# Optimization experiments

Hardware: AMD Instinct MI355X
Metric: run time of the kernel (lower is better)

## Reference

```python
import jax, jax.numpy as jnp
import numpy as np

EPS = 1e-08
K_N = 10
K_E = 10
F_DIM = 512
SCALE = F_DIM ** -0.5
N_NODES = 16384
N_EDGES = 2048


def layernorm(x, w, b):
    mu = x.mean(axis=-1, keepdims=True)
    var = x.var(axis=-1, keepdims=True)
    return (x - mu) * jax.lax.rsqrt(var + 1e-5) * w + b


def mask_attn(attn, k):
    # topk along last dim, scatter boolean mask, elementwise masking
    _, idx = jax.lax.top_k(attn, k)
    rows = jnp.arange(attn.shape[0])[:, None]
    mask = jnp.zeros(attn.shape, dtype=bool).at[rows, idx].set(True)
    return attn * mask


def setup_inputs() -> dict:
    key = jax.random.key(0)
    ks = jax.random.split(key, 12)
    d, h = F_DIM, 512  # hidden = max(f_dim, 128)
    w = 0.02  # weight init scale to keep softmax unsaturated
    return {
        'inputs': jax.random.normal(ks[0], (N_NODES, d), jnp.float32),
        'noise': jax.random.normal(ks[1], (N_EDGES, d), jnp.float32),
        'edges_mu': jax.random.normal(ks[2], (1, d), jnp.float32),
        'edges_logsigma': jnp.zeros((1, d), jnp.float32),
        'Wq': jax.random.normal(ks[3], (d, d), jnp.float32) * w,
        'bq': jnp.zeros((d,), jnp.float32),
        'Wk': jax.random.normal(ks[4], (d, d), jnp.float32) * w,
        'bk': jnp.zeros((d,), jnp.float32),
        'Wv': jax.random.normal(ks[5], (d, d), jnp.float32) * w,
        'bv': jnp.zeros((d,), jnp.float32),
        'W1': jax.random.normal(ks[6], (2 * d, h), jnp.float32) * w,
        'b1': jnp.zeros((h,), jnp.float32),
        'W2': jax.random.normal(ks[7], (h, d), jnp.float32) * w,
        'b2': jnp.zeros((d,), jnp.float32),
        'ln_in_w': jnp.ones((d,), jnp.float32),
        'ln_in_b': jnp.zeros((d,), jnp.float32),
        'ln_e_w': jnp.ones((d,), jnp.float32),
        'ln_e_b': jnp.zeros((d,), jnp.float32),
    }


def reference(inputs, noise, edges_mu, edges_logsigma, Wq, bq, Wk, bk, Wv, bv,
              W1, b1, W2, b2, ln_in_w, ln_in_b, ln_e_w, ln_e_b):
    relu = jax.nn.relu
    # slot init: mu + sigma * noise  -> [n_s, d]
    edges = edges_mu + jnp.exp(edges_logsigma) * noise
    x = layernorm(inputs, ln_in_w, ln_in_b)          # [n, d]
    k = relu(x @ Wk + bk)                            # [n, d]
    v = relu(x @ Wv + bv)                            # [n, d]
    # single iteration (iters=1)
    e = layernorm(edges, ln_e_w, ln_e_b)             # [n_s, d]
    q = relu(e @ Wq + bq)                            # [n_s, d]
    dots = (q @ k.T) * SCALE                         # [n_s, n]
    attn = jax.nn.softmax(dots, axis=1) + EPS
    attn = attn / attn.sum(axis=1, keepdims=True)
    attn = mask_attn(attn, K_N)
    updates = attn @ v                               # [n_s, d]
    e = jnp.concatenate([e, updates], axis=1)        # [n_s, 2d]
    e = relu(e @ W1 + b1) @ W2 + b2                  # mlp -> [n_s, d]
    q2 = x @ Wq + bq                                 # note: no activation here
    k2 = relu(e @ Wk + bk)                           # [n_s, d]
    dots2 = (q2 @ k2.T) * SCALE                      # [n, n_s]
    attn_v = jax.nn.softmax(dots2, axis=1)
    H = mask_attn(attn_v, K_E)
    return e, H, dots2
```

## Files before the change

kernel.cpp:

```cpp
#include <hip/hip_runtime.h>
#include <stdint.h>


#define NN 16384
#define NE 2048
#define TOPK 10

static const float SCALE_F = 0.04419417382415922f;
#define EPS_F 1e-8f

using bf16x8  = __attribute__((ext_vector_type(8))) __bf16;
using floatx4 = __attribute__((ext_vector_type(4))) float;

__device__ __forceinline__ unsigned f_as_u(float f) {
  union { float f; unsigned u; } v; v.f = f; return v.u;
}
__device__ __forceinline__ float u_as_f(unsigned u) {
  union { unsigned u; float f; } v; v.u = u; return v.f;
}
__device__ __forceinline__ unsigned short f2bf(float f) {
  unsigned u = f_as_u(f);
  unsigned r = u + 0x7fffu + ((u >> 16) & 1u);
  return (unsigned short)(r >> 16);
}
__device__ __forceinline__ float bf2f(unsigned short h) {
  return u_as_f(((unsigned)h) << 16);
}

__device__ __forceinline__ void glds16(const unsigned short* g, unsigned short* l) {
  __builtin_amdgcn_global_load_lds(
      (const __attribute__((address_space(1))) unsigned int*)g,
      (__attribute__((address_space(3))) unsigned int*)l, 16, 0, 0);
}

__device__ __forceinline__ unsigned fkey(float f) {
  unsigned u = f_as_u(f);
  return (u & 0x80000000u) ? ~u : (u | 0x80000000u);
}
__device__ __forceinline__ float funkey(unsigned k) {
  unsigned u = (k & 0x80000000u) ? (k ^ 0x80000000u) : ~k;
  return u_as_f(u);
}
__device__ __forceinline__ unsigned long long packkc(float v, int col) {
  return ((unsigned long long)fkey(v) << 32) | (unsigned)(~(unsigned)col);
}
__device__ __forceinline__ int unpack_col(unsigned long long w) {
  return (int)(~(unsigned)(w & 0xFFFFFFFFull));
}
__device__ __forceinline__ float unpack_val(unsigned long long w) {
  return funkey((unsigned)(w >> 32));
}
__device__ __forceinline__ unsigned long long shfl_xor_u64(unsigned long long x, int m) {
  unsigned lo = (unsigned)x, hi = (unsigned)(x >> 32);
  lo = __shfl_xor(lo, m, 64);
  hi = __shfl_xor(hi, m, 64);
  return ((unsigned long long)hi << 32) | lo;
}

__global__ void transpose_cast_kernel(const float* __restrict__ src,
                                      unsigned short* __restrict__ dhi,
                                      unsigned short* __restrict__ dlo,
                                      int K, int N) {
  __shared__ float tile[32][33];
  int n0 = blockIdx.x * 32, k0 = blockIdx.y * 32;
  int tx = threadIdx.x, ty = threadIdx.y;
  for (int r = ty; r < 32; r += 8)
    tile[r][tx] = src[(size_t)(k0 + r) * N + n0 + tx];
  __syncthreads();
  for (int r = ty; r < 32; r += 8) {
    float v = tile[tx][r];
    size_t o = (size_t)(n0 + r) * K + k0 + tx;
    unsigned short h = f2bf(v);
    dhi[o] = h;
    if (dlo) dlo[o] = f2bf(v - bf2f(h));
  }
}

__global__ void transpose_cast3_kernel(const float* __restrict__ s0,
                                       const float* __restrict__ s1,
                                       const float* __restrict__ s2,
                                       unsigned short* __restrict__ dhi) {
  __shared__ float tile[32][33];
  const float* src = blockIdx.z == 0 ? s0 : (blockIdx.z == 1 ? s1 : s2);
  unsigned short* d = dhi + (size_t)blockIdx.z * 512 * 512;
  int n0 = blockIdx.x * 32, k0 = blockIdx.y * 32;
  int tx = threadIdx.x, ty = threadIdx.y;
  for (int r = ty; r < 32; r += 8)
    tile[r][tx] = src[(size_t)(k0 + r) * 512 + n0 + tx];
  __syncthreads();
  for (int r = ty; r < 32; r += 8)
    d[(size_t)(n0 + r) * 512 + k0 + tx] = f2bf(tile[tx][r]);
}

__device__ __forceinline__ float block_sum_256(float v, float* sm4) {
#pragma unroll
  for (int off = 32; off; off >>= 1) v += __shfl_down(v, off, 64);
  __syncthreads();
  if ((threadIdx.x & 63) == 0) sm4[threadIdx.x >> 6] = v;
  __syncthreads();
  return (sm4[0] + sm4[1]) + (sm4[2] + sm4[3]);
}

__global__ __launch_bounds__(256) void ln_x_kernel(
    const float* __restrict__ in, const float* __restrict__ w,
    const float* __restrict__ b, unsigned short* __restrict__ out_hi) {
  __shared__ float sm4[4];
  int row = blockIdx.x, tid = threadIdx.x;
  const float* r = in + (size_t)row * 512;
  float x0 = r[tid], x1 = r[tid + 256];
  float mu = block_sum_256(x0 + x1, sm4) * (1.0f / 512.0f);
  float d0 = x0 - mu, d1 = x1 - mu;
  float var = block_sum_256(d0 * d0 + d1 * d1, sm4) * (1.0f / 512.0f);
  float rs = rsqrtf(var + 1e-5f);
  out_hi[(size_t)row * 512 + tid]       = f2bf(d0 * rs * w[tid] + b[tid]);
  out_hi[(size_t)row * 512 + tid + 256] = f2bf(d1 * rs * w[tid + 256] + b[tid + 256]);
}

__global__ __launch_bounds__(256) void ln_e_kernel(
    const float* __restrict__ noise, const float* __restrict__ mu_e,
    const float* __restrict__ ls_e, const float* __restrict__ w,
    const float* __restrict__ b, unsigned short* __restrict__ e1_hi,
    unsigned short* __restrict__ e1_lo) {
  __shared__ float sm4[4];
  int row = blockIdx.x, tid = threadIdx.x;
  const float* r = noise + (size_t)row * 512;
  float x0 = mu_e[tid] + expf(ls_e[tid]) * r[tid];
  float x1 = mu_e[tid + 256] + expf(ls_e[tid + 256]) * r[tid + 256];
  float mu = block_sum_256(x0 + x1, sm4) * (1.0f / 512.0f);
  float d0 = x0 - mu, d1 = x1 - mu;
  float var = block_sum_256(d0 * d0 + d1 * d1, sm4) * (1.0f / 512.0f);
  float rs = rsqrtf(var + 1e-5f);
  float y0 = d0 * rs * w[tid] + b[tid];
  float y1 = d1 * rs * w[tid + 256] + b[tid + 256];
  size_t o = (size_t)row * 1024;
  unsigned short h0 = f2bf(y0), h1 = f2bf(y1);
  e1_hi[o + tid] = h0;             e1_lo[o + tid] = f2bf(y0 - bf2f(h0));
  e1_hi[o + tid + 256] = h1;       e1_lo[o + tid + 256] = f2bf(y1 - bf2f(h1));
}

#define GEMM128_CORE(A_, B_, bm_, bn_, acc_)                                   \
  __shared__ __align__(16) unsigned short As[128 * 32];                        \
  __shared__ __align__(16) unsigned short Bs[128 * 32];                        \
  {                                                                            \
    const unsigned short* gA0 = (A_) + ((bm_) + (tid >> 2)) * 512 + ((tid & 3) << 3); \
    const unsigned short* gA1 = gA0 + 64 * 512;                                \
    const unsigned short* gB0 = (B_) + ((bn_) + (tid >> 2)) * 512 + ((tid & 3) << 3); \
    const unsigned short* gB1 = gB0 + 64 * 512;                                \
    unsigned short* dA0 = &As[wave * 512];                                     \
    unsigned short* dA1 = &As[2048 + wave * 512];                              \
    unsigned short* dB0 = &Bs[wave * 512];                                     \
    unsigned short* dB1 = &Bs[2048 + wave * 512];                              \
    for (int k0 = 0; k0 < 512; k0 += 32) {                                     \
      glds16(gA0 + k0, dA0);                                                   \
      glds16(gA1 + k0, dA1);                                                   \
      glds16(gB0 + k0, dB0);                                                   \
      glds16(gB1 + k0, dB1);                                                   \
      __syncthreads();                                                         \
      bf16x8 af0 = *(const bf16x8*)&As[(wave * 32 + lrow) * 32 + quad * 8];    \
      bf16x8 af1 = *(const bf16x8*)&As[(wave * 32 + 16 + lrow) * 32 + quad * 8]; \
      _Pragma("unroll")                                                        \
      for (int t = 0; t < 8; ++t) {                                            \
        bf16x8 bfr = *(const bf16x8*)&Bs[(t * 16 + lrow) * 32 + quad * 8];     \
        acc_[0][t] = __builtin_amdgcn_mfma_f32_16x16x32_bf16(af0, bfr, acc_[0][t], 0, 0, 0); \
        acc_[1][t] = __builtin_amdgcn_mfma_f32_16x16x32_bf16(af1, bfr, acc_[1][t], 0, 0, 0); \
      }                                                                        \
      __syncthreads();                                                         \
    }                                                                          \
  }

__global__ __launch_bounds__(256) void gemm128_dots_kernel(
    const unsigned short* __restrict__ A, const unsigned short* __restrict__ B,
    float alpha, float* __restrict__ C, int ldc) {
  int tid = threadIdx.x, wave = tid >> 6, lane = tid & 63;
  int lrow = lane & 15, quad = lane >> 4;
  size_t bm = (size_t)blockIdx.x * 128, bn = (size_t)blockIdx.y * 128;
  floatx4 zero4 = {0.f, 0.f, 0.f, 0.f};
  floatx4 acc[2][8];
#pragma unroll
  for (int i = 0; i < 2; ++i)
#pragma unroll
    for (int t = 0; t < 8; ++t) acc[i][t] = zero4;
  GEMM128_CORE(A, B, bm, bn, acc)
#pragma unroll
  for (int i = 0; i < 2; ++i) {
    size_t row0 = bm + wave * 32 + i * 16 + quad * 4;
#pragma unroll
    for (int t = 0; t < 8; ++t) {
      int col = (int)bn + t * 16 + lrow;
#pragma unroll
      for (int r = 0; r < 4; ++r)
        C[(row0 + r) * (size_t)ldc + col] = acc[i][t][r] * alpha;
    }
  }
}

__global__ __launch_bounds__(256) void gemm128_kvq_kernel(
    const unsigned short* __restrict__ A, const unsigned short* __restrict__ B,
    const float* __restrict__ bk, const float* __restrict__ bv,
    const float* __restrict__ bq,
    unsigned short* __restrict__ khi, unsigned short* __restrict__ vhi,
    unsigned short* __restrict__ q2hi) {
  int tid = threadIdx.x, wave = tid >> 6, lane = tid & 63;
  int lrow = lane & 15, quad = lane >> 4;
  size_t bm = (size_t)blockIdx.x * 128, bn = (size_t)blockIdx.y * 128;
  floatx4 zero4 = {0.f, 0.f, 0.f, 0.f};
  floatx4 acc[2][8];
#pragma unroll
  for (int i = 0; i < 2; ++i)
#pragma unroll
    for (int t = 0; t < 8; ++t) acc[i][t] = zero4;
  GEMM128_CORE(A, B, bm, bn, acc)
  int mat = (int)(bn >> 9);
  int colbase = (int)(bn & 511);
  const float* bias = mat == 0 ? bk : (mat == 1 ? bv : bq);
  unsigned short* dst = mat == 0 ? khi : (mat == 1 ? vhi : q2hi);
  bool relu = mat < 2;
#pragma unroll
  for (int i = 0; i < 2; ++i) {
    size_t row0 = bm + wave * 32 + i * 16 + quad * 4;
#pragma unroll
    for (int t = 0; t < 8; ++t) {
      int col = colbase + t * 16 + lrow;
      float bvv = bias[col];
#pragma unroll
      for (int r = 0; r < 4; ++r) {
        float v = acc[i][t][r] + bvv;
        if (relu) v = fmaxf(v, 0.0f);
        dst[(row0 + r) * 512 + col] = f2bf(v);
      }
    }
  }
}

template <bool SPLIT, bool RELU, bool HAS_BIAS, bool WF32, bool WHI, bool WLO>
__global__ __launch_bounds__(256) void gemm64_kernel(
    const unsigned short* __restrict__ Ahi, const unsigned short* __restrict__ Alo, int lda,
    const unsigned short* __restrict__ Bhi, const unsigned short* __restrict__ Blo, int K,
    const float* __restrict__ bias, float alpha,
    float* __restrict__ Cf, int ldc,
    unsigned short* __restrict__ Chi, unsigned short* __restrict__ Clo, int ldcb) {
  __shared__ __align__(16) unsigned short AsH[64 * 32];
  __shared__ __align__(16) unsigned short BsH[64 * 32];
  __shared__ __align__(16) unsigned short AsL[64 * 32];
  __shared__ __align__(16) unsigned short BsL[64 * 32];
  int tid = threadIdx.x, wave = tid >> 6, lane = tid & 63;
  int lrow = lane & 15, quad = lane >> 4;
  size_t bm = (size_t)blockIdx.x * 64, bn = (size_t)blockIdx.y * 64;
  int row = tid >> 2, off = (tid & 3) << 3;
  size_t aoff = (bm + row) * (size_t)lda + off;
  size_t boff = (bn + row) * (size_t)K + off;

  floatx4 zero4 = {0.f, 0.f, 0.f, 0.f};
  floatx4 acc[4];
#pragma unroll
  for (int t = 0; t < 4; ++t) acc[t] = zero4;

  for (int k0 = 0; k0 < K; k0 += 32) {
    uint4 ah = *(const uint4*)(Ahi + aoff + k0);
    uint4 bh = *(const uint4*)(Bhi + boff + k0);
    uint4 al, bl;
    if (SPLIT) {
      al = *(const uint4*)(Alo + aoff + k0);
      bl = *(const uint4*)(Blo + boff + k0);
    }
    __syncthreads();
    *(uint4*)&AsH[tid * 8] = ah;
    *(uint4*)&BsH[tid * 8] = bh;
    if (SPLIT) {
      *(uint4*)&AsL[tid * 8] = al;
      *(uint4*)&BsL[tid * 8] = bl;
    }
    __syncthreads();
    int ai = (wave * 16 + lrow) * 32 + quad * 8;
    bf16x8 aH = *(const bf16x8*)&AsH[ai];
    bf16x8 aL;
    if (SPLIT) aL = *(const bf16x8*)&AsL[ai];
#pragma unroll
    for (int t = 0; t < 4; ++t) {
      int bi = (t * 16 + lrow) * 32 + quad * 8;
      bf16x8 bH = *(const bf16x8*)&BsH[bi];
      acc[t] = __builtin_amdgcn_mfma_f32_16x16x32_bf16(aH, bH, acc[t], 0, 0, 0);
      if (SPLIT) {
        bf16x8 bL = *(const bf16x8*)&BsL[bi];
        acc[t] = __builtin_amdgcn_mfma_f32_16x16x32_bf16(aH, bL, acc[t], 0, 0, 0);
        acc[t] = __builtin_amdgcn_mfma_f32_16x16x32_bf16(aL, bH, acc[t], 0, 0, 0);
      }
    }
  }
  size_t row0 = bm + wave * 16 + quad * 4;
#pragma unroll
  for (int t = 0; t < 4; ++t) {
    int col = (int)bn + t * 16 + lrow;
    float bv = HAS_BIAS ? bias[col] : 0.0f;
#pragma unroll
    for (int r = 0; r < 4; ++r) {
      float v = acc[t][r] * alpha + bv;
      if (RELU) v = fmaxf(v, 0.0f);
      if (WF32) Cf[(row0 + r) * (size_t)ldc + col] = v;
      if (WHI) {
        unsigned short h = f2bf(v);
        Chi[(row0 + r) * (size_t)ldcb + col] = h;
        if (WLO) Clo[(row0 + r) * (size_t)ldcb + col] = f2bf(v - bf2f(h));
      }
    }
  }
}

#define INSERT4(lv, li, v, col)                                   \
  do {                                                            \
    if ((v) > lv[3]) {                                            \
      float cv_ = (v); int ci_ = (col);                           \
      _Pragma("unroll")                                           \
      for (int j_ = 0; j_ < 4; ++j_) {                            \
        bool sw_ = (cv_ > lv[j_]);                                \
        float tv_ = sw_ ? lv[j_] : cv_;                           \
        int ti_ = sw_ ? li[j_] : ci_;                              \
        lv[j_] = sw_ ? cv_ : lv[j_];                              \
        li[j_] = sw_ ? ci_ : li[j_];                              \
        cv_ = tv_; ci_ = ti_;                                     \
      }                                                           \
    }                                                             \
  } while (0)

__global__ __launch_bounds__(256) void attn1_kernel(
    const float* __restrict__ dots,
    const unsigned short* __restrict__ vhi,
    unsigned short* __restrict__ e1_hi, unsigned short* __restrict__ e1_lo) {
  __shared__ float sm_m[4], sm_s[4];
  __shared__ unsigned long long wbest[4];
  __shared__ unsigned long long wkey_s[TOPK];

  int tid = threadIdx.x, wave = tid >> 6, lane = tid & 63;
  int rowi = blockIdx.x;
  const float4* r4 = (const float4*)(dots + (size_t)rowi * NN);

  float lv[4]; int li[4];
#pragma unroll
  for (int j = 0; j < 4; ++j) { lv[j] = -INFINITY; li[j] = 0x7fffffff; }
  unsigned long long selmask = 0ull;
  int taken = 0;

  float m_loc = -INFINITY, s_loc = 0.0f;
  for (int i = 0; i < 16; ++i) {
    float4 q = r4[tid + (i << 8)];
#pragma unroll
    for (int c = 0; c < 4; ++c) {
      float v = (&q.x)[c];
      int col = ((tid + (i << 8)) << 2) + c;
      if (v > m_loc) {
        s_loc = s_loc * __expf(m_loc - v) + 1.0f;
        m_loc = v;
      } else {
        s_loc += __expf(v - m_loc);
      }
      INSERT4(lv, li, v, col);
    }
  }
#pragma unroll
  for (int sft = 32; sft; sft >>= 1) {
    float om = __shfl_xor(m_loc, sft, 64);
    float os = __shfl_xor(s_loc, sft, 64);
    float M = fmaxf(m_loc, om);
    s_loc = s_loc * __expf(m_loc - M) + os * __expf(om - M);
    m_loc = M;
  }
  if (lane == 0) { sm_m[wave] = m_loc; sm_s[wave] = s_loc; }
  __syncthreads();
  float M = fmaxf(fmaxf(sm_m[0], sm_m[1]), fmaxf(sm_m[2], sm_m[3]));
  float Z = sm_s[0] * __expf(sm_m[0] - M) + sm_s[1] * __expf(sm_m[1] - M) +
            sm_s[2] * __expf(sm_m[2] - M) + sm_s[3] * __expf(sm_m[3] - M);

  for (int rnd = 0; rnd < TOPK; ++rnd) {
    unsigned long long key;
    if (taken < 4) {
      key = packkc(lv[0], li[0]);
    } else {
      key = 0ull;
      for (int i = 0; i < 16; ++i) {
        float4 q = r4[tid + (i << 8)];
#pragma unroll
        for (int c = 0; c < 4; ++c) {
          int sl = i * 4 + c;
          if (!((selmask >> sl) & 1ull)) {
            int col = ((tid + (i << 8)) << 2) + c;
            unsigned long long kk = packkc((&q.x)[c], col);
            if (kk > key) key = kk;
          }
        }
      }
    }
#pragma unroll
    for (int sft = 32; sft; sft >>= 1) {
      unsigned long long ok = shfl_xor_u64(key, sft);
      if (ok > key) key = ok;
    }
    if (lane == 0) wbest[wave] = key;
    __syncthreads();
    unsigned long long w = wbest[0];
    if (wbest[1] > w) w = wbest[1];
    if (wbest[2] > w) w = wbest[2];
    if (wbest[3] > w) w = wbest[3];
    if (tid == 0) wkey_s[rnd] = w;
    int wcol = unpack_col(w);
    if (((wcol >> 2) & 255) == tid) {
      int sl = ((wcol >> 10) << 2) | (wcol & 3);
      selmask |= (1ull << sl);
      if (taken < 4) {
#pragma unroll
        for (int j = 0; j < 3; ++j) { lv[j] = lv[j + 1]; li[j] = li[j + 1]; }
      }
      ++taken;
    }
    __syncthreads();
  }

  const float inv_den = 1.0f / (1.0f + (float)NN * EPS_F);
  float invZ = 1.0f / Z;
  float u0 = 0.f, u1 = 0.f;
#pragma unroll
  for (int j = 0; j < TOPK; ++j) {
    unsigned long long w = wkey_s[j];
    int col = unpack_col(w);
    float val = unpack_val(w);
    float a = (__expf(val - M) * invZ + EPS_F) * inv_den;
    const unsigned short* vr = vhi + (size_t)col * 512;
    u0 += a * bf2f(vr[tid]);
    u1 += a * bf2f(vr[tid + 256]);
  }
  size_t o = (size_t)rowi * 1024 + 512;
  unsigned short h0 = f2bf(u0), h1 = f2bf(u1);
  e1_hi[o + tid] = h0;             e1_lo[o + tid] = f2bf(u0 - bf2f(h0));
  e1_hi[o + tid + 256] = h1;       e1_lo[o + tid + 256] = f2bf(u1 - bf2f(h1));
}

__global__ __launch_bounds__(256) void attn2_kernel(const float* __restrict__ dots2,
                                                    float* __restrict__ Hout) {
  int tid = threadIdx.x, wave = tid >> 6, lane = tid & 63;
  int rowi = blockIdx.x * 4 + wave;
  const float4* r4 = (const float4*)(dots2 + (size_t)rowi * NE);

  float d[32];
  float m = -INFINITY;
#pragma unroll
  for (int i = 0; i < 8; ++i) {
    float4 q = r4[lane + (i << 6)];
#pragma unroll
    for (int c = 0; c < 4; ++c) {
      d[i * 4 + c] = (&q.x)[c];
      m = fmaxf(m, d[i * 4 + c]);
    }
  }
#pragma unroll
  for (int sft = 32; sft; sft >>= 1) m = fmaxf(m, __shfl_xor(m, sft, 64));

  float s = 0.f;
#pragma unroll
  for (int j = 0; j < 32; ++j) { d[j] = __expf(d[j] - m); s += d[j]; }
#pragma unroll
  for (int sft = 32; sft; sft >>= 1) s += __shfl_xor(s, sft, 64);
  float invZ = 1.0f / s;

  float lv[4]; int li[4];
#pragma unroll
  for (int j = 0; j < 4; ++j) { lv[j] = -INFINITY; li[j] = 0x7fffffff; }
#pragma unroll
  for (int i = 0; i < 8; ++i) {
#pragma unroll
    for (int c = 0; c < 4; ++c) {
      int col = ((lane + (i << 6)) << 2) + c;
      INSERT4(lv, li, d[i * 4 + c], col);
    }
  }

  unsigned selmask = 0;
  int taken = 0;
  for (int rnd = 0; rnd < TOPK; ++rnd) {
    unsigned long long key;
    if (taken < 4) {
      key = packkc(lv[0], li[0]);
    } else {
      key = 0ull;
#pragma unroll
      for (int j = 0; j < 32; ++j) {
        if (!((selmask >> j) & 1u)) {
          int col = ((lane + ((j >> 2) << 6)) << 2) + (j & 3);
          unsigned long long kk = packkc(d[j], col);
          if (kk > key) key = kk;
        }
      }
    }
#pragma unroll
    for (int sft = 32; sft; sft >>= 1) {
      unsigned long long ok = shfl_xor_u64(key, sft);
      if (ok > key) key = ok;
    }
    int wcol = unpack_col(key);
    if (((wcol >> 2) & 63) == lane) {
      int sl = ((wcol >> 8) << 2) | (wcol & 3);
      selmask |= (1u << sl);
      if (taken < 4) {
#pragma unroll
        for (int j = 0; j < 3; ++j) { lv[j] = lv[j + 1]; li[j] = li[j + 1]; }
      }
      ++taken;
    }
  }

  float* hr = Hout + (size_t)rowi * NE;
#pragma unroll
  for (int i = 0; i < 8; ++i) {
    float4 o;
#pragma unroll
    for (int c = 0; c < 4; ++c) {
      int sl = i * 4 + c;
      (&o.x)[c] = ((selmask >> sl) & 1u) ? d[sl] * invZ : 0.0f;
    }
    ((float4*)hr)[lane + (i << 6)] = o;
  }
}

extern "C" void kernel_launch(void* const* d_in, const int* in_sizes, int n_in,
                              void* d_out, int out_size, void* d_ws, size_t ws_size,
                              hipStream_t stream) {
  (void)in_sizes; (void)n_in; (void)out_size; (void)ws_size;
  const float* inputs  = (const float*)d_in[0];
  const float* noise   = (const float*)d_in[1];
  const float* edges_mu = (const float*)d_in[2];
  const float* edges_ls = (const float*)d_in[3];
  const float* Wq = (const float*)d_in[4];
  const float* bq = (const float*)d_in[5];
  const float* Wk = (const float*)d_in[6];
  const float* bk = (const float*)d_in[7];
  const float* Wv = (const float*)d_in[8];
  const float* bv = (const float*)d_in[9];
  const float* W1 = (const float*)d_in[10];
  const float* b1 = (const float*)d_in[11];
  const float* W2 = (const float*)d_in[12];
  const float* b2 = (const float*)d_in[13];
  const float* ln_in_w = (const float*)d_in[14];
  const float* ln_in_b = (const float*)d_in[15];
  const float* ln_e_w = (const float*)d_in[16];
  const float* ln_e_b = (const float*)d_in[17];

  float* out_e  = (float*)d_out;
  float* out_H  = out_e + (size_t)NE * 512;
  float* out_d2 = out_H + (size_t)NN * NE;

  const size_t MB = 1024 * 1024;
  unsigned char* hb = (unsigned char*)out_H;
  unsigned short* x_hi  = (unsigned short*)(hb);
  unsigned short* k_hi  = (unsigned short*)(hb + 16 * MB);
  unsigned short* v_hi  = (unsigned short*)(hb + 32 * MB);
  unsigned short* q2_hi = (unsigned short*)(hb + 48 * MB);
  unsigned short* WcatT = (unsigned short*)(hb + 64 * MB);
  unsigned short* W1Th  = (unsigned short*)(hb + 66 * MB);
  unsigned short* W1Tl  = (unsigned short*)(hb + 67 * MB);
  unsigned short* W2Th  = (unsigned short*)(hb + 68 * MB);
  unsigned short* W2Tl  = (unsigned short*)(hb + 68 * MB + 512 * 1024);
  unsigned short* e1_hi = (unsigned short*)(hb + 70 * MB);
  unsigned short* e1_lo = (unsigned short*)(hb + 74 * MB);
  unsigned short* q_hi  = (unsigned short*)(hb + 78 * MB);
  unsigned short* h_hi  = (unsigned short*)(hb + 80 * MB);
  unsigned short* h_lo  = (unsigned short*)(hb + 82 * MB);
  unsigned short* e_hi  = (unsigned short*)(hb + 84 * MB);
  unsigned short* WkT   = WcatT;
  unsigned short* WqT   = WcatT + (size_t)1024 * 512;
  float* dots = out_d2;
  unsigned short* k2_hi = (unsigned short*)d_ws;

  dim3 tb(256);
  dim3 t32(32, 8);

  transpose_cast3_kernel<<<dim3(16, 16, 3), t32, 0, stream>>>(Wk, Wv, Wq, WcatT);
  transpose_cast_kernel<<<dim3(16, 32), t32, 0, stream>>>(W1, W1Th, W1Tl, 1024, 512);
  transpose_cast_kernel<<<dim3(16, 16), t32, 0, stream>>>(W2, W2Th, W2Tl, 512, 512);

  ln_x_kernel<<<NN, tb, 0, stream>>>(inputs, ln_in_w, ln_in_b, x_hi);
  ln_e_kernel<<<NE, tb, 0, stream>>>(noise, edges_mu, edges_ls, ln_e_w, ln_e_b, e1_hi, e1_lo);

  gemm128_kvq_kernel<<<dim3(128, 12), tb, 0, stream>>>(
      x_hi, WcatT, bk, bv, bq, k_hi, v_hi, q2_hi);
  gemm64_kernel<false, true, true, false, true, false><<<dim3(32, 8), tb, 0, stream>>>(
      e1_hi, nullptr, 1024, WqT, nullptr, 512, bq, 1.f, nullptr, 0, q_hi, nullptr, 512);
  gemm128_dots_kernel<<<dim3(16, 128), tb, 0, stream>>>(q_hi, k_hi, SCALE_F, dots, NN);
  attn1_kernel<<<NE, tb, 0, stream>>>(dots, v_hi, e1_hi, e1_lo);
  gemm64_kernel<true, true, true, false, true, true><<<dim3(32, 8), tb, 0, stream>>>(
      e1_hi, e1_lo, 1024, W1Th, W1Tl, 1024, b1, 1.f, nullptr, 0, h_hi, h_lo, 512);
  gemm64_kernel<true, false, true, true, true, false><<<dim3(32, 8), tb, 0, stream>>>(
      h_hi, h_lo, 512, W2Th, W2Tl, 512, b2, 1.f, out_e, 512, e_hi, nullptr, 512);
  gemm64_kernel<false, true, true, false, true, false><<<dim3(32, 8), tb, 0, stream>>>(
      e_hi, nullptr, 512, WkT, nullptr, 512, bk, 1.f, nullptr, 0, k2_hi, nullptr, 512);
  gemm128_dots_kernel<<<dim3(128, 16), tb, 0, stream>>>(q2_hi, k2_hi, SCALE_F, out_d2, NE);
  attn2_kernel<<<NN / 4, tb, 0, stream>>>(out_d2, out_H);
}
```

Before: 570.8 us.

## Replace 128-tile GEMMs with pipelined 256x256 swizzled-LDS MFMA kernel

Swaps the 128x128 bf16 GEMM core for a 256x256 tile, 512-thread kernel with a multi-slot LDS ring (128KB). It overlaps global-to-LDS loads with MFMA work through explicit vmcnt waits, raised wave priority and an XOR-swizzled LDS layout that avoids bank conflicts. The grid is remapped to 1D with a chiplet-aware block index swizzle. The larger tile raises data reuse, at the cost of fewer blocks and high register/LDS use that limits occupancy.

```diff
diff --git a/kernel.cpp b/kernel.cpp
--- a/kernel.cpp
+++ b/kernel.cpp
@@ -138,93 +138,155 @@
   e1_hi[o + tid + 256] = h1;       e1_lo[o + tid + 256] = f2bf(y1 - bf2f(h1));
 }
 
-#define GEMM128_CORE(A_, B_, bm_, bn_, acc_)                                   \
-  __shared__ __align__(16) unsigned short As[128 * 32];                        \
-  __shared__ __align__(16) unsigned short Bs[128 * 32];                        \
+
+#define NOVM ((void)0)
+#define VM2 asm volatile("s_waitcnt vmcnt(2)" ::: "memory")
+#define VM0 asm volatile("s_waitcnt vmcnt(0)" ::: "memory")
+#define NOSTAGE ((void)0)
+
+#define STAGE(G_, rowbase_, kb_, slotptr_)                                     \
+  { const unsigned short* g0_ =                                                \
+        (G_) + ((rowbase_) + (size_t)sr0) * 512 + (kb_) + sc0;                 \
+    const unsigned short* g1_ =                                                \
+        (G_) + ((rowbase_) + (size_t)sr1) * 512 + (kb_) + sc1;                 \
+    glds16(g0_, (unsigned short*)((char*)(slotptr_) + wave * 1024));           \
+    glds16(g1_, (unsigned short*)((char*)(slotptr_) + 8192 + wave * 1024)); }
+
+#define PHASE(IM0_, IN0_, ASL_, BSL_, STAGE_STMT_, VM_)                        \
   {                                                                            \
-    const unsigned short* gA0 = (A_) + ((bm_) + (tid >> 2)) * 512 + ((tid & 3) << 3); \
-    const unsigned short* gA1 = gA0 + 64 * 512;                                \
-    const unsigned short* gB0 = (B_) + ((bn_) + (tid >> 2)) * 512 + ((tid & 3) << 3); \
-    const unsigned short* gB1 = gB0 + 64 * 512;                                \
-    unsigned short* dA0 = &As[wave * 512];                                     \
-    unsigned short* dA1 = &As[2048 + wave * 512];                              \
-    unsigned short* dB0 = &Bs[wave * 512];                                     \
-    unsigned short* dB1 = &Bs[2048 + wave * 512];                              \
-    for (int k0 = 0; k0 < 512; k0 += 32) {                                     \
-      glds16(gA0 + k0, dA0);                                                   \
-      glds16(gA1 + k0, dA1);                                                   \
-      glds16(gB0 + k0, dB0);                                                   \
-      glds16(gB1 + k0, dB1);                                                   \
-      __syncthreads();                                                         \
-      bf16x8 af0 = *(const bf16x8*)&As[(wave * 32 + lrow) * 32 + quad * 8];    \
-      bf16x8 af1 = *(const bf16x8*)&As[(wave * 32 + 16 + lrow) * 32 + quad * 8]; \
-      _Pragma("unroll")                                                        \
-      for (int t = 0; t < 8; ++t) {                                            \
-        bf16x8 bfr = *(const bf16x8*)&Bs[(t * 16 + lrow) * 32 + quad * 8];     \
-        acc_[0][t] = __builtin_amdgcn_mfma_f32_16x16x32_bf16(af0, bfr, acc_[0][t], 0, 0, 0); \
-        acc_[1][t] = __builtin_amdgcn_mfma_f32_16x16x32_bf16(af1, bfr, acc_[1][t], 0, 0, 0); \
+    const char* Ap_ = ldsA_c + (ASL_) * 16384;                                 \
+    const char* Bp_ = ldsB_c + (BSL_) * 16384;                                 \
+    bf16x8 af_[4][2], bg_[2][2];                                               \
+    _Pragma("unroll") for (int i_ = 0; i_ < 4; ++i_) {                         \
+      af_[i_][0] = *(const bf16x8*)(Ap_ + aoff0 + i_ * 4096);                  \
+      af_[i_][1] = *(const bf16x8*)(Ap_ + aoff1 + i_ * 4096);                  \
+    }                                                                          \
+    _Pragma("unroll") for (int j_ = 0; j_ < 2; ++j_) {                         \
+      bg_[j_][0] = *(const bf16x8*)(Bp_ + boff0 + j_ * 8192);                  \
+      bg_[j_][1] = *(const bf16x8*)(Bp_ + boff1 + j_ * 8192);                  \
+    }                                                                          \
+    STAGE_STMT_;                                                               \
+    VM_;                                                                       \
+    __builtin_amdgcn_sched_barrier(0);                                         \
+    __builtin_amdgcn_s_barrier();                                              \
+    __builtin_amdgcn_sched_barrier(0);                                         \
+    __builtin_amdgcn_s_setprio(1);                                             \
+    _Pragma("unroll") for (int i_ = 0; i_ < 4; ++i_)                           \
+      _Pragma("unroll") for (int j_ = 0; j_ < 2; ++j_) {                       \
+        acc[(IM0_) + i_][(IN0_) + j_] =                                        \
+            __builtin_amdgcn_mfma_f32_16x16x32_bf16(                           \
+                af_[i_][0], bg_[j_][0], acc[(IM0_) + i_][(IN0_) + j_], 0, 0, 0);\
+        acc[(IM0_) + i_][(IN0_) + j_] =                                        \
+            __builtin_amdgcn_mfma_f32_16x16x32_bf16(                           \
+                af_[i_][1], bg_[j_][1], acc[(IM0_) + i_][(IN0_) + j_], 0, 0, 0);\
       }                                                                        \
-      __syncthreads();                                                         \
+    __builtin_amdgcn_s_setprio(0);                                             \
+  }
+
+#define GEMM256_CORE(A_, B_)                                                   \
+  __shared__ __align__(16) char lds_all[131072];                               \
+  char* ldsA_s = lds_all;                                                      \
+  char* ldsB_s = lds_all + 65536;                                              \
+  const char* ldsA_c = lds_all;                                                \
+  const char* ldsB_c = lds_all + 65536;                                        \
+  int tid = threadIdx.x, wave = tid >> 6, lane = tid & 63;                     \
+  int lrow = lane & 15, quad = lane >> 4;                                      \
+  int wfm = wave >> 2, wfn = wave & 3;                                         \
+  int smask = ((lrow >> 2) & 3) << 5;                                          \
+  int aoff0 = (wfm * 16 + lrow) * 128 + ((quad * 16) ^ smask);                 \
+  int aoff1 = aoff0 ^ 64;                                                      \
+  int boff0 = (wfn * 16 + lrow) * 128 + ((quad * 16) ^ smask);                 \
+  int boff1 = boff0 ^ 64;                                                      \
+  int p0_ = tid * 16, l0_ = p0_ ^ (((p0_ >> 9) & 3) << 5);                     \
+  int sr0 = l0_ >> 7, sc0 = (l0_ & 127) >> 1;                                  \
+  int p1_ = 8192 + tid * 16, l1_ = p1_ ^ (((p1_ >> 9) & 3) << 5);              \
+  int sr1 = l1_ >> 7, sc1 = (l1_ & 127) >> 1;                                  \
+  floatx4 acc[8][4];                                                           \
+  { floatx4 z4_ = {0.f, 0.f, 0.f, 0.f};                                        \
+    _Pragma("unroll") for (int i_ = 0; i_ < 8; ++i_)                           \
+      _Pragma("unroll") for (int j_ = 0; j_ < 4; ++j_) acc[i_][j_] = z4_; }    \
+        \
+  STAGE(A_, bm, 0, ldsA_s)                                                     \
+  STAGE(B_, bn, 0, ldsB_s)                                                     \
+  STAGE(A_, bm + 128, 0, ldsA_s + 16384)                                       \
+  STAGE(B_, bn + 128, 0, ldsB_s + 16384)                                       \
+  STAGE(A_, bm, 64, ldsA_s + 32768)                                            \
+  VM2;                                                                         \
+  __builtin_amdgcn_sched_barrier(0);                                           \
+  __builtin_amdgcn_s_barrier();                                                \
+  __builtin_amdgcn_sched_barrier(0);                                           \
+  for (int t2 = 0; t2 < 8; t2 += 2) {                                          \
+    int kn = (t2 + 1) * 64, kn2 = (t2 + 2) * 64, kn3 = (t2 + 3) * 64;          \
+                                    \
+    PHASE(0, 0, 0, 0, STAGE(B_, bn, kn, ldsB_s + 32768), NOVM)                 \
+    PHASE(0, 2, 0, 1, STAGE(A_, bm + 128, kn, ldsA_s + 49152), NOVM)           \
+    PHASE(4, 0, 1, 0, STAGE(B_, bn + 128, kn, ldsB_s + 49152), NOVM)           \
+    if (t2 < 6) {                                                              \
+      PHASE(4, 2, 1, 1, STAGE(A_, bm, kn2, ldsA_s), VM2)                       \
+                                   \
+      PHASE(0, 0, 2, 2, STAGE(B_, bn, kn2, ldsB_s), NOVM)                      \
+      PHASE(0, 2, 2, 3, STAGE(A_, bm + 128, kn2, ldsA_s + 16384), NOVM)        \
+      PHASE(4, 0, 3, 2, STAGE(B_, bn + 128, kn2, ldsB_s + 16384), NOVM)        \
+      PHASE(4, 2, 3, 3, STAGE(A_, bm, kn3, ldsA_s + 32768), VM2)               \
+    } else {                                                                   \
+      PHASE(4, 2, 1, 1, NOSTAGE, VM0)                                          \
+      PHASE(0, 0, 2, 2, NOSTAGE, NOVM)                                         \
+      PHASE(0, 2, 2, 3, NOSTAGE, NOVM)                                         \
+      PHASE(4, 0, 3, 2, NOSTAGE, NOVM)                                         \
+      PHASE(4, 2, 3, 3, NOSTAGE, NOVM)                                         \
     }                                                                          \
-  }
-
-__global__ __launch_bounds__(256) void gemm128_dots_kernel(
+    (void)kn3;                                                                 \
+  }
+
+__global__ __launch_bounds__(512, 2) void gemm256_dots_kernel(
     const unsigned short* __restrict__ A, const unsigned short* __restrict__ B,
-    float alpha, float* __restrict__ C, int ldc) {
-  int tid = threadIdx.x, wave = tid >> 6, lane = tid & 63;
-  int lrow = lane & 15, quad = lane >> 4;
-  size_t bm = (size_t)blockIdx.x * 128, bn = (size_t)blockIdx.y * 128;
-  floatx4 zero4 = {0.f, 0.f, 0.f, 0.f};
-  floatx4 acc[2][8];
-#pragma unroll
-  for (int i = 0; i < 2; ++i)
-#pragma unroll
-    for (int t = 0; t < 8; ++t) acc[i][t] = zero4;
-  GEMM128_CORE(A, B, bm, bn, acc)
-#pragma unroll
-  for (int i = 0; i < 2; ++i) {
-    size_t row0 = bm + wave * 32 + i * 16 + quad * 4;
-#pragma unroll
-    for (int t = 0; t < 8; ++t) {
-      int col = (int)bn + t * 16 + lrow;
+    float alpha, float* __restrict__ C, int ldc, int ntiles) {
+  int nwg = (int)gridDim.x;
+  int bid = (int)blockIdx.x;
+  int wg = (bid & 7) * (nwg >> 3) + (bid >> 3);
+  size_t bm = (size_t)(wg / ntiles) * 256;
+  size_t bn = (size_t)(wg % ntiles) * 256;
+  GEMM256_CORE(A, B)
+#pragma unroll
+  for (int im = 0; im < 8; ++im) {
+    size_t row0 = bm + im * 32 + wfm * 16 + quad * 4;
+#pragma unroll
+    for (int in = 0; in < 4; ++in) {
+      size_t col = bn + in * 64 + wfn * 16 + lrow;
 #pragma unroll
       for (int r = 0; r < 4; ++r)
-        C[(row0 + r) * (size_t)ldc + col] = acc[i][t][r] * alpha;
-    }
-  }
-}
-
-__global__ __launch_bounds__(256) void gemm128_kvq_kernel(
+        C[(row0 + r) * (size_t)ldc + col] = acc[im][in][r] * alpha;
+    }
+  }
+}
+
+__global__ __launch_bounds__(512, 2) void gemm256_kvq_kernel(
     const unsigned short* __restrict__ A, const unsigned short* __restrict__ B,
     const float* __restrict__ bk, const float* __restrict__ bv,
     const float* __restrict__ bq,
     unsigned short* __restrict__ khi, unsigned short* __restrict__ vhi,
-    unsigned short* __restrict__ q2hi) {
-  int tid = threadIdx.x, wave = tid >> 6, lane = tid & 63;
-  int lrow = lane & 15, quad = lane >> 4;
-  size_t bm = (size_t)blockIdx.x * 128, bn = (size_t)blockIdx.y * 128;
-  floatx4 zero4 = {0.f, 0.f, 0.f, 0.f};
-  floatx4 acc[2][8];
-#pragma unroll
-  for (int i = 0; i < 2; ++i)
-#pragma unroll
-    for (int t = 0; t < 8; ++t) acc[i][t] = zero4;
-  GEMM128_CORE(A, B, bm, bn, acc)
+    unsigned short* __restrict__ q2hi, int ntiles) {
+  int nwg = (int)gridDim.x;
+  int bid = (int)blockIdx.x;
+  int wg = (bid & 7) * (nwg >> 3) + (bid >> 3);
+  size_t bm = (size_t)(wg / ntiles) * 256;
+  size_t bn = (size_t)(wg % ntiles) * 256;
+  GEMM256_CORE(A, B)
   int mat = (int)(bn >> 9);
   int colbase = (int)(bn & 511);
   const float* bias = mat == 0 ? bk : (mat == 1 ? bv : bq);
   unsigned short* dst = mat == 0 ? khi : (mat == 1 ? vhi : q2hi);
   bool relu = mat < 2;
 #pragma unroll
-  for (int i = 0; i < 2; ++i) {
-    size_t row0 = bm + wave * 32 + i * 16 + quad * 4;
-#pragma unroll
-    for (int t = 0; t < 8; ++t) {
-      int col = colbase + t * 16 + lrow;
+  for (int im = 0; im < 8; ++im) {
+    size_t row0 = bm + im * 32 + wfm * 16 + quad * 4;
+#pragma unroll
+    for (int in = 0; in < 4; ++in) {
+      int col = colbase + in * 64 + wfn * 16 + lrow;
       float bvv = bias[col];
 #pragma unroll
       for (int r = 0; r < 4; ++r) {
-        float v = acc[i][t][r] + bvv;
+        float v = acc[im][in][r] + bvv;
         if (relu) v = fmaxf(v, 0.0f);
         dst[(row0 + r) * 512 + col] = f2bf(v);
       }
@@ -578,11 +640,12 @@
   ln_x_kernel<<<NN, tb, 0, stream>>>(inputs, ln_in_w, ln_in_b, x_hi);
   ln_e_kernel<<<NE, tb, 0, stream>>>(noise, edges_mu, edges_ls, ln_e_w, ln_e_b, e1_hi, e1_lo);
 
-  gemm128_kvq_kernel<<<dim3(128, 12), tb, 0, stream>>>(
-      x_hi, WcatT, bk, bv, bq, k_hi, v_hi, q2_hi);
+  gemm256_kvq_kernel<<<dim3(384), dim3(512), 0, stream>>>(
+      x_hi, WcatT, bk, bv, bq, k_hi, v_hi, q2_hi, 6);
   gemm64_kernel<false, true, true, false, true, false><<<dim3(32, 8), tb, 0, stream>>>(
       e1_hi, nullptr, 1024, WqT, nullptr, 512, bq, 1.f, nullptr, 0, q_hi, nullptr, 512);
-  gemm128_dots_kernel<<<dim3(16, 128), tb, 0, stream>>>(q_hi, k_hi, SCALE_F, dots, NN);
+  gemm256_dots_kernel<<<dim3(512), dim3(512), 0, stream>>>(
+      q_hi, k_hi, SCALE_F, dots, NN, 64);
   attn1_kernel<<<NE, tb, 0, stream>>>(dots, v_hi, e1_hi, e1_lo);
   gemm64_kernel<true, true, true, false, true, true><<<dim3(32, 8), tb, 0, stream>>>(
       e1_hi, e1_lo, 1024, W1Th, W1Tl, 1024, b1, 1.f, nullptr, 0, h_hi, h_lo, 512);
@@ -590,6 +653,7 @@
       h_hi, h_lo, 512, W2Th, W2Tl, 512, b2, 1.f, out_e, 512, e_hi, nullptr, 512);
   gemm64_kernel<false, true, true, false, true, false><<<dim3(32, 8), tb, 0, stream>>>(
       e_hi, nullptr, 512, WkT, nullptr, 512, bk, 1.f, nullptr, 0, k2_hi, nullptr, 512);
-  gemm128_dots_kernel<<<dim3(128, 16), tb, 0, stream>>>(q2_hi, k2_hi, SCALE_F, out_d2, NE);
+  gemm256_dots_kernel<<<dim3(512), dim3(512), 0, stream>>>(
+      q2_hi, k2_hi, SCALE_F, out_d2, NE, 8);
   attn2_kernel<<<NN / 4, tb, 0, stream>>>(out_d2, out_H);
 }
```

Result: slower. 910.4 us (+59.5%).

## Stage GEMM epilogues through LDS for vector stores and map blocks to XCD panels

Applied to the files above, without the earlier changes.

The 128x128 GEMM kernels now write their accumulator tiles into shared memory and read them back as row-contiguous 16-byte chunks. The goal is coalesced float4/uint4 global stores in place of scattered scalar stores. They also move to a 1D grid, remapping block IDs so that each XCD (blockIdx mod 8) works on a contiguous panel of the shared operand, which should improve L2 reuse across the chiplets. The cost is extra LDS traffic and barriers in the epilogue, and the dots kernel needs more shared memory, which may reduce occupancy.

```diff
diff --git a/kernel.cpp b/kernel.cpp
--- a/kernel.cpp
+++ b/kernel.cpp
@@ -138,9 +138,9 @@
   e1_hi[o + tid + 256] = h1;       e1_lo[o + tid + 256] = f2bf(y1 - bf2f(h1));
 }
 
-#define GEMM128_CORE(A_, B_, bm_, bn_, acc_)                                   \
-  __shared__ __align__(16) unsigned short As[128 * 32];                        \
-  __shared__ __align__(16) unsigned short Bs[128 * 32];                        \
+#define GEMM128_CORE(A_, B_, bm_, bn_, acc_, SMEM_)                            \
+  unsigned short* As = (unsigned short*)(SMEM_);                               \
+  unsigned short* Bs = (unsigned short*)(SMEM_) + 4096;                        \
   {                                                                            \
     const unsigned short* gA0 = (A_) + ((bm_) + (tid >> 2)) * 512 + ((tid & 3) << 3); \
     const unsigned short* gA1 = gA0 + 64 * 512;                                \
@@ -168,29 +168,45 @@
     }                                                                          \
   }
 
+#define XCD_PANEL_MAP(mt_, nt_, owns_m_)                                       \
+  int bid = (int)blockIdx.x, xcd = bid & 7, idx = bid >> 3;                    \
+  int per = ((owns_m_) ? (mt_) : (nt_)) >> 3;                                  \
+  int pa = idx % per, pb = idx / per;                                          \
+  size_t bm = (size_t)((owns_m_) ? (xcd * per + pa) : pb) * 128;               \
+  size_t bn = (size_t)((owns_m_) ? pb : (xcd * per + pa)) * 128;
+
 __global__ __launch_bounds__(256) void gemm128_dots_kernel(
     const unsigned short* __restrict__ A, const unsigned short* __restrict__ B,
-    float alpha, float* __restrict__ C, int ldc) {
+    float alpha, float* __restrict__ C, int ldc, int mt, int nt, int owns_m) {
+  __shared__ __align__(16) char smem[33792];
   int tid = threadIdx.x, wave = tid >> 6, lane = tid & 63;
   int lrow = lane & 15, quad = lane >> 4;
-  size_t bm = (size_t)blockIdx.x * 128, bn = (size_t)blockIdx.y * 128;
+  XCD_PANEL_MAP(mt, nt, owns_m)
   floatx4 zero4 = {0.f, 0.f, 0.f, 0.f};
   floatx4 acc[2][8];
 #pragma unroll
   for (int i = 0; i < 2; ++i)
 #pragma unroll
     for (int t = 0; t < 8; ++t) acc[i][t] = zero4;
-  GEMM128_CORE(A, B, bm, bn, acc)
+  GEMM128_CORE(A, B, bm, bn, acc, smem)
+  __syncthreads();
+  float* wb = (float*)smem + wave * (16 * 132);
 #pragma unroll
   for (int i = 0; i < 2; ++i) {
-    size_t row0 = bm + wave * 32 + i * 16 + quad * 4;
-#pragma unroll
-    for (int t = 0; t < 8; ++t) {
-      int col = (int)bn + t * 16 + lrow;
+#pragma unroll
+    for (int t = 0; t < 8; ++t)
 #pragma unroll
       for (int r = 0; r < 4; ++r)
-        C[(row0 + r) * (size_t)ldc + col] = acc[i][t][r] * alpha;
-    }
+        wb[(quad * 4 + r) * 132 + t * 16 + lrow] = acc[i][t][r] * alpha;
+    __syncthreads();
+    size_t rowbase = bm + wave * 32 + i * 16;
+#pragma unroll
+    for (int p = 0; p < 8; ++p) {
+      int rr = p * 2 + (lane >> 5);
+      float4 v = *(const float4*)&wb[rr * 132 + ((lane & 31) << 2)];
+      *(float4*)&C[(rowbase + rr) * (size_t)ldc + bn + ((lane & 31) << 2)] = v;
+    }
+    __syncthreads();
   }
 }
 
@@ -200,35 +216,45 @@
     const float* __restrict__ bq,
     unsigned short* __restrict__ khi, unsigned short* __restrict__ vhi,
     unsigned short* __restrict__ q2hi) {
+  __shared__ __align__(16) char smem[17408];
   int tid = threadIdx.x, wave = tid >> 6, lane = tid & 63;
   int lrow = lane & 15, quad = lane >> 4;
-  size_t bm = (size_t)blockIdx.x * 128, bn = (size_t)blockIdx.y * 128;
+  XCD_PANEL_MAP(128, 12, 1)
   floatx4 zero4 = {0.f, 0.f, 0.f, 0.f};
   floatx4 acc[2][8];
 #pragma unroll
   for (int i = 0; i < 2; ++i)
 #pragma unroll
     for (int t = 0; t < 8; ++t) acc[i][t] = zero4;
-  GEMM128_CORE(A, B, bm, bn, acc)
+  GEMM128_CORE(A, B, bm, bn, acc, smem)
   int mat = (int)(bn >> 9);
   int colbase = (int)(bn & 511);
   const float* bias = mat == 0 ? bk : (mat == 1 ? bv : bq);
   unsigned short* dst = mat == 0 ? khi : (mat == 1 ? vhi : q2hi);
   bool relu = mat < 2;
+  __syncthreads();
+  unsigned short* wb = (unsigned short*)smem + wave * (16 * 136);
 #pragma unroll
   for (int i = 0; i < 2; ++i) {
-    size_t row0 = bm + wave * 32 + i * 16 + quad * 4;
 #pragma unroll
     for (int t = 0; t < 8; ++t) {
-      int col = colbase + t * 16 + lrow;
-      float bvv = bias[col];
+      float bvv = bias[colbase + t * 16 + lrow];
 #pragma unroll
       for (int r = 0; r < 4; ++r) {
         float v = acc[i][t][r] + bvv;
         if (relu) v = fmaxf(v, 0.0f);
-        dst[(row0 + r) * 512 + col] = f2bf(v);
-      }
-    }
+        wb[(quad * 4 + r) * 136 + t * 16 + lrow] = f2bf(v);
+      }
+    }
+    __syncthreads();
+    size_t rowbase = bm + wave * 32 + i * 16;
+#pragma unroll
+    for (int p = 0; p < 4; ++p) {
+      int rr = p * 4 + (lane >> 4);
+      uint4 v = *(const uint4*)&wb[rr * 136 + ((lane & 15) << 3)];
+      *(uint4*)&dst[(rowbase + rr) * 512 + colbase + ((lane & 15) << 3)] = v;
+    }
+    __syncthreads();
   }
 }
 
@@ -578,11 +604,12 @@
   ln_x_kernel<<<NN, tb, 0, stream>>>(inputs, ln_in_w, ln_in_b, x_hi);
   ln_e_kernel<<<NE, tb, 0, stream>>>(noise, edges_mu, edges_ls, ln_e_w, ln_e_b, e1_hi, e1_lo);
 
-  gemm128_kvq_kernel<<<dim3(128, 12), tb, 0, stream>>>(
+  gemm128_kvq_kernel<<<dim3(1536), tb, 0, stream>>>(
       x_hi, WcatT, bk, bv, bq, k_hi, v_hi, q2_hi);
   gemm64_kernel<false, true, true, false, true, false><<<dim3(32, 8), tb, 0, stream>>>(
       e1_hi, nullptr, 1024, WqT, nullptr, 512, bq, 1.f, nullptr, 0, q_hi, nullptr, 512);
-  gemm128_dots_kernel<<<dim3(16, 128), tb, 0, stream>>>(q_hi, k_hi, SCALE_F, dots, NN);
+  gemm128_dots_kernel<<<dim3(2048), tb, 0, stream>>>(
+      q_hi, k_hi, SCALE_F, dots, NN, 16, 128, 0);
   attn1_kernel<<<NE, tb, 0, stream>>>(dots, v_hi, e1_hi, e1_lo);
   gemm64_kernel<true, true, true, false, true, true><<<dim3(32, 8), tb, 0, stream>>>(
       e1_hi, e1_lo, 1024, W1Th, W1Tl, 1024, b1, 1.f, nullptr, 0, h_hi, h_lo, 512);
@@ -590,6 +617,7 @@
       h_hi, h_lo, 512, W2Th, W2Tl, 512, b2, 1.f, out_e, 512, e_hi, nullptr, 512);
   gemm64_kernel<false, true, true, false, true, false><<<dim3(32, 8), tb, 0, stream>>>(
       e_hi, nullptr, 512, WkT, nullptr, 512, bk, 1.f, nullptr, 0, k2_hi, nullptr, 512);
-  gemm128_dots_kernel<<<dim3(128, 16), tb, 0, stream>>>(q2_hi, k2_hi, SCALE_F, out_d2, NE);
+  gemm128_dots_kernel<<<dim3(2048), tb, 0, stream>>>(
+      q2_hi, k2_hi, SCALE_F, out_d2, NE, 128, 16, 1);
   attn2_kernel<<<NN / 4, tb, 0, stream>>>(out_d2, out_H);
 }
```

New measurement: 571.3 us. Within noise of the previous version (+0.1%).
